# Performance work log

Measured on AMD Instinct MI355X. Metric: run time of the kernel, lower is better.

## Reference

```python
import jax, jax.numpy as jnp
from jax import lax
import numpy as np
import math

B, T, D_IN, H, L, NDIR = 32, 512, 1024, 512, 2, 2


def setup_inputs() -> dict:
    key = jax.random.key(0)
    ks = jax.random.split(key, 5)
    std = 1.0 / math.sqrt(H)  # torch init: uniform(-std, std)
    u = lambda k, shape: jax.random.uniform(k, shape, jnp.float32, -std, std)
    return {
        "x": jax.random.normal(ks[0], (B, T, D_IN), jnp.float32),
        "Wx": u(ks[1], (L, NDIR, D_IN, 4 * H)),   # x2h weight (in, 4H)
        "bx": u(ks[2], (L, NDIR, 4 * H)),
        "Wh": u(ks[3], (L, NDIR, H, 4 * H)),      # h2h weight (H, 4H)
        "bh": u(ks[4], (L, NDIR, 4 * H)),
    }


def _lstm_dir(xs, Wx, bx, Wh, bh):
    """xs: [T,B,Din]; returns hs [T,B,H], (hT, cT)."""
    # precompute input projection for all timesteps (one big GEMM)
    gx = jnp.einsum('tbd,dg->tbg', xs, Wx) + bx + bh  # [T,B,4H]
    h0 = jnp.zeros((xs.shape[1], Wh.shape[0]), xs.dtype)

    def step(carry, gx_t):
        h, c = carry
        gates = gx_t + h @ Wh  # [B,4H]
        i, f, g, o = jnp.split(gates, 4, axis=-1)  # torch chunk order: i,f,g,o
        i = jax.nn.sigmoid(i)
        f = jax.nn.sigmoid(f)
        g = jnp.tanh(g)
        o = jax.nn.sigmoid(o)
        c = c * f + i * g
        h = o * jnp.tanh(c)
        return (h, c), h

    (hT, cT), hs = lax.scan(step, (h0, h0), gx)
    return hs, hT, cT


def reference(x, Wx, bx, Wh, bh):
    # x: [B,T,D_IN] (batch_first) -> time-major
    inputs = jnp.swapaxes(x, 0, 1)  # [T,B,D]
    h_list, c_list = [], []
    for layer in range(L):
        outs_dirs = []
        for d in range(NDIR):
            xs = inputs if d == 0 else inputs[::-1]
            hs, hT, cT = _lstm_dir(xs, Wx[layer, d], bx[layer, d], Wh[layer, d], bh[layer, d])
            outs_dirs.append(hs if d == 0 else hs[::-1])
            h_list.append(hT)
            c_list.append(cT)
        inputs = jnp.concatenate(outs_dirs, axis=-1)  # [T,B,2H] (dropout=0 / eval)
    output = jnp.swapaxes(inputs, 0, 1)  # [B,T,2H]
    h_n = jnp.stack(h_list)  # [L*NDIR, B, H]
    c_n = jnp.stack(c_list)
    return output, h_n, c_n
```

## Files before the change

### kernel.cpp

```cpp
#include <hip/hip_runtime.h>
#include <hip/hip_bf16.h>

#define DEV __device__ __forceinline__

typedef __bf16 bf16;
typedef __bf16 bf16x8 __attribute__((ext_vector_type(8)));
typedef float f32x4 __attribute__((ext_vector_type(4)));
typedef int i32x4 __attribute__((ext_vector_type(4)));
typedef unsigned int u32;
typedef unsigned long long u64;

#define BB 32
#define TT 512
#define DIN 1024
#define HH 512
#define G4 2048
#define MM (TT*BB)

DEV float sigmf(float x){ return 1.0f/(1.0f + __expf(-x)); }
DEV float tanhfast(float x){ return 1.0f - 2.0f/(__expf(2.0f*x)+1.0f); }

DEV void gload16(const void* g, void* l){
  __builtin_amdgcn_global_load_lds((const __attribute__((address_space(1))) void*)g,
                                   (__attribute__((address_space(3))) void*)l, 16, 0, 0);
}

DEV i32x4 cload16(const void* p){
  i32x4 v;
  asm volatile("global_load_dwordx4 %0, %1, off sc0 sc1"
               : "=&v"(v) : "v"(p) : "memory");
  return v;
}
DEV void cstore8(void* p, u64 v){
  asm volatile("global_store_dwordx2 %0, %1, off sc0 sc1"
               :: "v"(p), "v"(v) : "memory");
}
DEV void waitvm0(){ asm volatile("s_waitcnt vmcnt(0)" ::: "memory"); }

__global__ void k_dbg(float* out, float v){ out[0] = v; }

__global__ void k_prep_bias(const float* __restrict__ bx, const float* __restrict__ bh,
                            float* __restrict__ bsum){
  int gid = blockIdx.x*256 + threadIdx.x;
  if (gid < 4*G4) bsum[gid] = bx[gid] + bh[gid];
}

__global__ void k_xswz(const float* __restrict__ x, bf16* __restrict__ xs){
  int gid = blockIdx.x*256 + threadIdx.x;
  int r = gid >> 7, kc = gid & 127;
  int b = r & 31, t = r >> 5;
  const float* px = x + ((size_t)b*TT + t)*DIN + kc*8;
  float4 v0 = *(const float4*)px;
  float4 v1 = *(const float4*)(px+4);
  bf16x8 o;
  o[0]=(bf16)v0.x; o[1]=(bf16)v0.y; o[2]=(bf16)v0.z; o[3]=(bf16)v0.w;
  o[4]=(bf16)v1.x; o[5]=(bf16)v1.y; o[6]=(bf16)v1.z; o[7]=(bf16)v1.w;
  *(bf16x8*)(xs + (size_t)r*DIN + ((kc ^ (r&7))<<3)) = o;
}

__global__ void k_twx(const float* __restrict__ Wx, bf16* __restrict__ Wxt){
  int ld = blockIdx.z;
  int k0 = blockIdx.x*64, n0 = blockIdx.y*64;
  const float* in = Wx + (size_t)ld*DIN*G4;
  bf16* outp = Wxt + (size_t)ld*G4*DIN;
  __shared__ float tile[64][68];
  int tid = threadIdx.x;
  #pragma unroll
  for (int rr=0; rr<4; rr++){
    int row = rr*16 + (tid>>4); int c4 = (tid&15)*4;
    float4 v = *(const float4*)(in + (size_t)(k0+row)*G4 + n0 + c4);
    *(float4*)&tile[row][c4] = v;
  }
  __syncthreads();
  #pragma unroll
  for (int uu=0; uu<2; uu++){
    int u = uu*256 + tid;
    int nn = u>>3, ck = u&7;
    bf16x8 o;
    #pragma unroll
    for (int j=0;j<8;j++) o[j] = (bf16)tile[ck*8+j][nn];
    int ncol = n0 + nn;
    int kcg = (k0>>3) + ck;
    *(bf16x8*)(outp + (size_t)ncol*DIN + ((size_t)(kcg ^ (ncol&7))<<3)) = o;
  }
}

__global__ void k_twh(const float* __restrict__ Wh, bf16* __restrict__ Whb){
  int ld = blockIdx.z;
  int k0 = blockIdx.x*64, n0 = blockIdx.y*64;
  const float* in = Wh + (size_t)ld*HH*G4;
  bf16* outp = Whb + (size_t)ld*G4*HH;
  __shared__ float tile[64][68];
  int tid = threadIdx.x;
  #pragma unroll
  for (int rr=0; rr<4; rr++){
    int row = rr*16 + (tid>>4); int c4 = (tid&15)*4;
    float4 v = *(const float4*)(in + (size_t)(k0+row)*G4 + n0 + c4);
    *(float4*)&tile[row][c4] = v;
  }
  __syncthreads();
  #pragma unroll
  for (int uu=0; uu<2; uu++){
    int u = uu*256 + tid;
    int nn = u>>3, ck = u&7;
    bf16x8 o;
    #pragma unroll
    for (int j=0;j<8;j++) o[j] = (bf16)tile[ck*8+j][nn];
    int n = n0 + nn;
    int q = n >> 9, rem = n & 511;
    int s = rem >> 4, wq = (rem >> 2) & 3, hcv = rem & 3;
    int cc = s*64 + wq*16 + q*4 + hcv;
    *(bf16x8*)(outp + (size_t)cc*HH + k0 + ck*8) = o;
  }
}

__launch_bounds__(256, 1)
__global__ void k_gemmp(const bf16* __restrict__ A, const bf16* __restrict__ Bw,
                        const float* __restrict__ bias, bf16* __restrict__ out){
  int d = blockIdx.z;
  const bf16* Bp = Bw + (size_t)d*G4*DIN;
  const float* bp = bias + d*G4;
  bf16* op = out + (size_t)d*MM*G4;
  int n0 = blockIdx.x*128, r0 = blockIdx.y*128;
  int tid = threadIdx.x, lane = tid&63, w = tid>>6;
  __shared__ __align__(16) bf16 ldsA[128*64];
  __shared__ __align__(16) bf16 ldsB[128*64];
  f32x4 acc[4][4];
  #pragma unroll
  for (int i=0;i<4;i++)
    #pragma unroll
    for (int j=0;j<4;j++) acc[i][j] = (f32x4){0.f,0.f,0.f,0.f};
  int wm = w>>1, wn = w&1;
  for (int kt=0; kt<16; kt++){
    __syncthreads();
    #pragma unroll
    for (int p=0;p<4;p++){
      int seg = p*4 + w;
      int row = seg*8 + (lane>>3);
      int cch = lane&7;
      gload16(A  + (size_t)(r0+row)*DIN + kt*64 + cch*8, ldsA + seg*512);
      gload16(Bp + (size_t)(n0+row)*DIN + kt*64 + cch*8, ldsB + seg*512);
    }
    __syncthreads();
    #pragma unroll
    for (int ks=0; ks<2; ks++){
      bf16x8 af[4], bf_[4];
      #pragma unroll
      for (int at=0; at<4; at++){
        int row = wm*64 + at*16 + (lane&15);
        int ch = (ks*4 + (lane>>4)) ^ (row&7);
        af[at] = *(const bf16x8*)(ldsA + row*64 + ch*8);
      }
      #pragma unroll
      for (int bt=0; bt<4; bt++){
        int col = wn*64 + bt*16 + (lane&15);
        int ch = (ks*4 + (lane>>4)) ^ (col&7);
        bf_[bt] = *(const bf16x8*)(ldsB + col*64 + ch*8);
      }
      #pragma unroll
      for (int at=0; at<4; at++)
        #pragma unroll
        for (int bt=0; bt<4; bt++)
          acc[at][bt] = __builtin_amdgcn_mfma_f32_16x16x32_bf16(af[at], bf_[bt], acc[at][bt], 0,0,0);
    }
  }
  float bv[4];
  #pragma unroll
  for (int bt=0;bt<4;bt++) bv[bt] = bp[n0 + wn*64 + bt*16 + (lane&15)];
  int l4 = lane>>4;
  #pragma unroll
  for (int a=0; a<2; a++){
    int tt = (r0 + wm*64 + a*32) >> 5;
    #pragma unroll
    for (int bt=0; bt<4; bt++){
      int col = n0 + wn*64 + bt*16 + (lane&15);
      int q = col >> 9, rem = col & 511;
      int sD = rem >> 4, wR = (rem >> 2) & 3, hcD = rem & 3;
      int tIdx = wR*64 + l4*16 + q*4 + hcD;
      bf16x8 u8;
      #pragma unroll
      for (int j=0;j<4;j++) u8[j]   = (bf16)(acc[a*2][bt][j]   + bv[bt]);
      #pragma unroll
      for (int j=0;j<4;j++) u8[4+j] = (bf16)(acc[a*2+1][bt][j] + bv[bt]);
      *(bf16x8*)(op + (((size_t)tt*32 + sD)*256 + tIdx)*8) = u8;
    }
  }
}

__launch_bounds__(256, 1)
__global__ void k_rec(const bf16* __restrict__ Whb, const bf16* __restrict__ gx,
                      char* __restrict__ hbS, bf16* __restrict__ out0,
                      float* __restrict__ dout,
                      float* __restrict__ hn, float* __restrict__ cn, int layer){
  int tid = threadIdx.x, lane = tid&63, w = tid>>6;
  int d = blockIdx.x >> 5, s = blockIdx.x & 31;
  __shared__ __align__(16) bf16 hA[32*512];
  __shared__ __align__(8) unsigned short hP[4*128];
  const bf16* Wp = Whb + ((size_t)d*G4 + s*64 + w*16 + (lane&15))*HH;
  bf16x8 bfr[16];
  #pragma unroll
  for (int kk=0; kk<16; kk++) bfr[kk] = *(const bf16x8*)(Wp + kk*32 + (lane>>4)*8);
  float cst[2][4] = {{0,0,0,0},{0,0,0,0}};
  const bf16* gxD = gx + (size_t)d*MM*G4;
  int q = (lane>>2)&3, hc = lane&3;
  int m0 = lane&15;
  bool hi = (q >= 2), odd = (q & 1);

  for (int t=0; t<TT; t++){
    int tt = d ? (TT-1-t) : t;
    bf16x8 gv = *(const bf16x8*)(gxD + (((size_t)tt*32 + s)*256 + tid)*8);
    f32x4 acc0 = {0.f,0.f,0.f,0.f}, acc1 = {0.f,0.f,0.f,0.f};
    if (t > 0){
      const char* sS = hbS + ((size_t)(d*TT + (t-1)) << 15);
      i32x4 u[8];
      #pragma unroll
      for (int i=0;i<8;i++) u[i] = cload16(sS + ((size_t)(i*256 + tid) << 4));
      waitvm0();
      __builtin_amdgcn_sched_barrier(0);
      u32 valid = 0;
      #pragma unroll
      for (int i=0;i<8;i++){
        bool ok = (u[i].x != -1) && (u[i].y != -1) && (u[i].z != -1) && (u[i].w != -1);
        valid |= (ok ? 1u : 0u) << i;
      }
      while (__any(valid != 0xFFu)){
        __builtin_amdgcn_s_sleep(1);
        #pragma unroll
        for (int i=0;i<8;i++)
          if (!((valid>>i)&1)) u[i] = cload16(sS + ((size_t)(i*256 + tid) << 4));
        waitvm0();
        __builtin_amdgcn_sched_barrier(0);
        valid = 0;
        #pragma unroll
        for (int i=0;i<8;i++){
          bool ok = (u[i].x != -1) && (u[i].y != -1) && (u[i].z != -1) && (u[i].w != -1);
          valid |= (ok ? 1u : 0u) << i;
        }
      }
      __syncthreads();
      #pragma unroll
      for (int i=0;i<8;i++){
        int g = i*256 + tid; int row = g>>6, uc = g&63;
        *(i32x4*)((char*)hA + row*1024 + ((uc ^ (row&7))<<4)) = u[i];
      }
      __syncthreads();
      #pragma unroll
      for (int kk=0; kk<16; kk++){
        int ch = (kk*4 + (lane>>4)) ^ (m0&7);
        bf16x8 a0 = *(const bf16x8*)(hA + m0*HH + ch*8);
        bf16x8 a1 = *(const bf16x8*)(hA + (m0+16)*HH + ch*8);
        acc0 = __builtin_amdgcn_mfma_f32_16x16x32_bf16(a0, bfr[kk], acc0, 0,0,0);
        acc1 = __builtin_amdgcn_mfma_f32_16x16x32_bf16(a1, bfr[kk], acc1, 0,0,0);
      }
    }
    #pragma unroll
    for (int mt=0; mt<2; mt++){
      #pragma unroll
      for (int rg=0; rg<4; rg++){
        float gpre = (mt ? acc1[rg] : acc0[rg]) + (float)gv[mt*4+rg];
        float x4  = __shfl_xor(gpre, 4);
        float x8  = __shfl_xor(gpre, 8);
        float x12 = __shfl_xor(gpre, 12);
        float a04 = odd ? x4 : gpre,  b04 = odd ? gpre : x4;
        float a812 = odd ? x12 : x8,  b812 = odd ? x8 : x12;
        float ig = hi ? a812 : a04;
        float fg = hi ? b812 : b04;
        float gg = hi ? a04 : a812;
        float og = hi ? b04 : b812;
        float iv = sigmf(ig), fv = sigmf(fg), gv_ = tanhfast(gg), ov = sigmf(og);
        float c = cst[mt][rg]*fv + iv*gv_;
        cst[mt][rg] = c;
        float hvv = ov * tanhfast(c);
        if (q == 0){
          int b = mt*16 + (lane>>4)*4 + rg;
          hP[w*128 + b*4 + hc] = __builtin_bit_cast(unsigned short, (bf16)hvv);
          if (layer == 1)
            __builtin_nontemporal_store(hvv,
              dout + ((size_t)(b*TT + tt))*(2*HH) + d*HH + s*16 + w*4 + hc);
          if (t == TT-1)
            hn[((size_t)((layer*2+d)*BB + b))*HH + s*16 + w*4 + hc] = hvv;
        }
      }
    }
    if (t == TT-1 && q == 0){
      #pragma unroll
      for (int mt=0; mt<2; mt++)
        #pragma unroll
        for (int rg=0; rg<4; rg++){
          int b = mt*16 + (lane>>4)*4 + rg;
          cn[((size_t)((layer*2+d)*BB + b))*HH + s*16 + w*4 + hc] = cst[mt][rg];
        }
    }
    if (lane < 32){
      u64 d8 = *(const u64*)(hP + w*128 + lane*4);
      if (t < TT-1)
        cstore8(hbS + ((size_t)(d*TT + t) << 15) + (((size_t)lane*128 + s*4 + w) << 3), d8);
      if (layer == 0){
        int r = tt*BB + lane;
        int c = d*64 + s*2 + (w>>1);
        *(u64*)(out0 + (size_t)r*DIN + (size_t)(c ^ (r&7))*8 + (w&1)*4) = d8;
      }
    }
  }
}

extern "C" void kernel_launch(void* const* d_in, const int* in_sizes, int n_in,
                              void* d_out, int out_size, void* d_ws, size_t ws_size,
                              hipStream_t stream){
  const float* x  = (const float*)d_in[0];
  const float* Wx = (const float*)d_in[1];
  const float* bx = (const float*)d_in[2];
  const float* Wh = (const float*)d_in[3];
  const float* bh = (const float*)d_in[4];
  float* outp = (float*)d_out;
  char* ws = (char*)d_ws;

  const size_t szWxt  = (size_t)4*G4*DIN*2;
  const size_t szWhb  = (size_t)4*G4*HH*2;
  const size_t szBsum = (size_t)4*G4*4;
  const size_t szXO   = (size_t)MM*DIN*2;
  const size_t szHbS  = (size_t)2*TT*32768;
  const size_t szGx   = (size_t)2*MM*G4*2;

  size_t off = 0;
  auto take = [&](size_t b)->size_t{ size_t r = off; off = (off + b + 255) & ~(size_t)255; return r; };
  size_t oWxt = take(szWxt), oWhb = take(szWhb), oBsum = take(szBsum);
  size_t oXO  = take(szXO), oHbS = take(szHbS), oGx = take(szGx);
  if (off > ws_size){
    k_dbg<<<1, 1, 0, stream>>>(outp, (float)((double)ws_size / 1048576.0));
    return;
  }

  bf16* Wxt  = (bf16*)(ws + oWxt);
  bf16* Whb  = (bf16*)(ws + oWhb);
  float* bsum= (float*)(ws + oBsum);
  bf16* xo   = (bf16*)(ws + oXO);
  bf16* out0 = xo;
  char* hbS  = ws + oHbS;
  bf16* gx   = (bf16*)(ws + oGx);

  float* hn = outp + (size_t)BB*TT*2*HH;
  float* cn = hn + (size_t)4*BB*HH;

  k_prep_bias<<<32, 256, 0, stream>>>(bx, bh, bsum);
  k_xswz<<<(MM*128)/256, 256, 0, stream>>>(x, xo);
  k_twx<<<dim3(16,32,4), 256, 0, stream>>>(Wx, Wxt);
  k_twh<<<dim3(8,32,4), 256, 0, stream>>>(Wh, Whb);

  for (int layer=0; layer<2; layer++){
    hipMemsetAsync(hbS, 0xFF, szHbS, stream);
    const bf16* A = layer ? out0 : xo;
    k_gemmp<<<dim3(16,128,2), 256, 0, stream>>>(A, Wxt + (size_t)layer*2*G4*DIN,
                                                bsum + layer*2*G4, gx);
    k_rec<<<64, 256, 0, stream>>>(Whb + (size_t)layer*2*G4*HH, gx, hbS, out0,
                                  outp, hn, cn, layer);
  }
}
```

Baseline: 5.939 ms.

## Merge four recurrent slices per 1024-thread block and batch output stores

The recurrent LSTM kernel now runs 16 blocks of 1024 threads instead of 64 blocks of 256. Each block covers four hidden slices, so the previous-step hidden state is polled and staged into shared memory once per four slices, and fewer blocks take part in the cross-block flag handshake. Per-step output writes (the bf16 layer-0 activations and the fp32 final output) go into a shared buffer and are flushed every 8 steps as wider stores. This adds per-CU serial work, costs more for each 1024-thread barrier and adds an extra barrier every 8 steps. The final-layer output is now rebuilt from bf16-rounded values, which loses some precision.

```diff
diff --git a/kernel.cpp b/kernel.cpp
--- a/kernel.cpp
+++ b/kernel.cpp
@@ -187,16 +187,19 @@
   }
 }
 
-__launch_bounds__(256, 1)
+__launch_bounds__(1024, 4)
 __global__ void k_rec(const bf16* __restrict__ Whb, const bf16* __restrict__ gx,
                       char* __restrict__ hbS, bf16* __restrict__ out0,
                       float* __restrict__ dout,
                       float* __restrict__ hn, float* __restrict__ cn, int layer){
-  int tid = threadIdx.x, lane = tid&63, w = tid>>6;
-  int d = blockIdx.x >> 5, s = blockIdx.x & 31;
+  int tidp = threadIdx.x, lane = tidp&63, w = tidp>>6;
+  int d = blockIdx.x >> 3, wg = blockIdx.x & 7;
+  int s = wg*4 + (w>>2);
+  int wq = w & 3;
   __shared__ __align__(16) bf16 hA[32*512];
-  __shared__ __align__(8) unsigned short hP[4*128];
-  const bf16* Wp = Whb + ((size_t)d*G4 + s*64 + w*16 + (lane&15))*HH;
+  __shared__ __align__(8) unsigned short hP[16*128];
+  __shared__ __align__(8) u64 outbuf[8][32][16];
+  const bf16* Wp = Whb + ((size_t)d*G4 + s*64 + wq*16 + (lane&15))*HH;
   bf16x8 bfr[16];
   #pragma unroll
   for (int kk=0; kk<16; kk++) bfr[kk] = *(const bf16x8*)(Wp + kk*32 + (lane>>4)*8);
@@ -208,39 +211,39 @@
 
   for (int t=0; t<TT; t++){
     int tt = d ? (TT-1-t) : t;
-    bf16x8 gv = *(const bf16x8*)(gxD + (((size_t)tt*32 + s)*256 + tid)*8);
+    bf16x8 gv = *(const bf16x8*)(gxD + (((size_t)tt*32 + s)*256 + (wq*64 + lane))*8);
     f32x4 acc0 = {0.f,0.f,0.f,0.f}, acc1 = {0.f,0.f,0.f,0.f};
     if (t > 0){
       const char* sS = hbS + ((size_t)(d*TT + (t-1)) << 15);
-      i32x4 u[8];
-      #pragma unroll
-      for (int i=0;i<8;i++) u[i] = cload16(sS + ((size_t)(i*256 + tid) << 4));
+      i32x4 u[2];
+      #pragma unroll
+      for (int i=0;i<2;i++) u[i] = cload16(sS + ((size_t)(i*1024 + tidp) << 4));
       waitvm0();
       __builtin_amdgcn_sched_barrier(0);
       u32 valid = 0;
       #pragma unroll
-      for (int i=0;i<8;i++){
+      for (int i=0;i<2;i++){
         bool ok = (u[i].x != -1) && (u[i].y != -1) && (u[i].z != -1) && (u[i].w != -1);
         valid |= (ok ? 1u : 0u) << i;
       }
-      while (__any(valid != 0xFFu)){
+      while (__any(valid != 3u)){
         __builtin_amdgcn_s_sleep(1);
         #pragma unroll
-        for (int i=0;i<8;i++)
-          if (!((valid>>i)&1)) u[i] = cload16(sS + ((size_t)(i*256 + tid) << 4));
+        for (int i=0;i<2;i++)
+          if (!((valid>>i)&1)) u[i] = cload16(sS + ((size_t)(i*1024 + tidp) << 4));
         waitvm0();
         __builtin_amdgcn_sched_barrier(0);
         valid = 0;
         #pragma unroll
-        for (int i=0;i<8;i++){
+        for (int i=0;i<2;i++){
           bool ok = (u[i].x != -1) && (u[i].y != -1) && (u[i].z != -1) && (u[i].w != -1);
           valid |= (ok ? 1u : 0u) << i;
         }
       }
       __syncthreads();
       #pragma unroll
-      for (int i=0;i<8;i++){
-        int g = i*256 + tid; int row = g>>6, uc = g&63;
+      for (int i=0;i<2;i++){
+        int g = i*1024 + tidp; int row = g>>6, uc = g&63;
         *(i32x4*)((char*)hA + row*1024 + ((uc ^ (row&7))<<4)) = u[i];
       }
       __syncthreads();
@@ -274,11 +277,8 @@
         if (q == 0){
           int b = mt*16 + (lane>>4)*4 + rg;
           hP[w*128 + b*4 + hc] = __builtin_bit_cast(unsigned short, (bf16)hvv);
-          if (layer == 1)
-            __builtin_nontemporal_store(hvv,
-              dout + ((size_t)(b*TT + tt))*(2*HH) + d*HH + s*16 + w*4 + hc);
           if (t == TT-1)
-            hn[((size_t)((layer*2+d)*BB + b))*HH + s*16 + w*4 + hc] = hvv;
+            hn[((size_t)((layer*2+d)*BB + b))*HH + s*16 + wq*4 + hc] = hvv;
         }
       }
     }
@@ -288,17 +288,39 @@
         #pragma unroll
         for (int rg=0; rg<4; rg++){
           int b = mt*16 + (lane>>4)*4 + rg;
-          cn[((size_t)((layer*2+d)*BB + b))*HH + s*16 + w*4 + hc] = cst[mt][rg];
+          cn[((size_t)((layer*2+d)*BB + b))*HH + s*16 + wq*4 + hc] = cst[mt][rg];
         }
     }
     if (lane < 32){
       u64 d8 = *(const u64*)(hP + w*128 + lane*4);
       if (t < TT-1)
-        cstore8(hbS + ((size_t)(d*TT + t) << 15) + (((size_t)lane*128 + s*4 + w) << 3), d8);
-      if (layer == 0){
-        int r = tt*BB + lane;
-        int c = d*64 + s*2 + (w>>1);
-        *(u64*)(out0 + (size_t)r*DIN + (size_t)(c ^ (r&7))*8 + (w&1)*4) = d8;
+        cstore8(hbS + ((size_t)(d*TT + t) << 15) + (((size_t)lane*128 + s*4 + wq) << 3), d8);
+      outbuf[t&7][lane][w] = d8;
+    }
+    if ((t&7) == 7){
+      __syncthreads();
+      int tbase = t - 7;
+      #pragma unroll
+      for (int k2=0; k2<4; k2++){
+        int u2 = k2*1024 + tidp;
+        int st = u2>>9, rem = u2&511, b = rem>>4, un = rem&15;
+        int tl = tbase + st;
+        int ttl = d ? (TT-1-tl) : tl;
+        u64 d8 = outbuf[st][b][un];
+        int s2 = wg*4 + (un>>2), w2 = un&3;
+        if (layer == 0){
+          int r = ttl*BB + b;
+          int c = d*64 + s2*2 + (w2>>1);
+          *(u64*)(out0 + (size_t)r*DIN + (size_t)(c ^ (r&7))*8 + (w2&1)*4) = d8;
+        } else {
+          const unsigned short* hp2 = (const unsigned short*)&d8;
+          float4 f;
+          f.x = __builtin_bit_cast(float, (u32)hp2[0] << 16);
+          f.y = __builtin_bit_cast(float, (u32)hp2[1] << 16);
+          f.z = __builtin_bit_cast(float, (u32)hp2[2] << 16);
+          f.w = __builtin_bit_cast(float, (u32)hp2[3] << 16);
+          *(float4*)(dout + ((size_t)(b*TT + ttl))*(2*HH) + d*HH + s2*16 + w2*4) = f;
+        }
       }
     }
   }
@@ -352,7 +374,7 @@
     const bf16* A = layer ? out0 : xo;
     k_gemmp<<<dim3(16,128,2), 256, 0, stream>>>(A, Wxt + (size_t)layer*2*G4*DIN,
                                                 bsum + layer*2*G4, gx);
-    k_rec<<<64, 256, 0, stream>>>(Whb + (size_t)layer*2*G4*HH, gx, hbS, out0,
-                                  outp, hn, cn, layer);
-  }
-}
+    k_rec<<<16, 1024, 0, stream>>>(Whb + (size_t)layer*2*G4*HH, gx, hbS, out0,
+                                   outp, hn, cn, layer);
+  }
+}
```

Result: slower. 13.50 ms (+127.3%).

## Load recurrent h fragments directly from global into MFMA registers, skipping LDS staging

Applied to the files above, without the earlier changes.

Each wave now loads the previous-step hidden state straight from the global staging buffer into MFMA A-operand registers in fragment layout, instead of cooperatively loading into registers, writing to swizzled LDS, and re-reading. This removes two block barriers and the LDS round trip from the serial per-timestep critical path. In exchange, every wave redundantly fetches the full 32x512 h tile, four times the global/L2 traffic per block. It also raises register pressure (32 vector registers of 16 bytes) and weakens the staleness check to two words per fragment.

```diff
diff --git a/kernel.cpp b/kernel.cpp
--- a/kernel.cpp
+++ b/kernel.cpp
@@ -194,7 +194,6 @@
                       float* __restrict__ hn, float* __restrict__ cn, int layer){
   int tid = threadIdx.x, lane = tid&63, w = tid>>6;
   int d = blockIdx.x >> 5, s = blockIdx.x & 31;
-  __shared__ __align__(16) bf16 hA[32*512];
   __shared__ __align__(8) unsigned short hP[4*128];
   const bf16* Wp = Whb + ((size_t)d*G4 + s*64 + w*16 + (lane&15))*HH;
   bf16x8 bfr[16];
@@ -205,6 +204,7 @@
   int q = (lane>>2)&3, hc = lane&3;
   int m0 = lane&15;
   bool hi = (q >= 2), odd = (q & 1);
+  int boff = m0*1024 + (lane>>4)*16;
 
   for (int t=0; t<TT; t++){
     int tt = d ? (TT-1-t) : t;
@@ -212,45 +212,42 @@
     f32x4 acc0 = {0.f,0.f,0.f,0.f}, acc1 = {0.f,0.f,0.f,0.f};
     if (t > 0){
       const char* sS = hbS + ((size_t)(d*TT + (t-1)) << 15);
-      i32x4 u[8];
-      #pragma unroll
-      for (int i=0;i<8;i++) u[i] = cload16(sS + ((size_t)(i*256 + tid) << 4));
+      i32x4 fa[16], fb[16];
+      #pragma unroll
+      for (int kk=0; kk<16; kk++){
+        fa[kk] = cload16(sS + boff + kk*64);
+        fb[kk] = cload16(sS + boff + 16384 + kk*64);
+      }
       waitvm0();
       __builtin_amdgcn_sched_barrier(0);
-      u32 valid = 0;
-      #pragma unroll
-      for (int i=0;i<8;i++){
-        bool ok = (u[i].x != -1) && (u[i].y != -1) && (u[i].z != -1) && (u[i].w != -1);
-        valid |= (ok ? 1u : 0u) << i;
-      }
-      while (__any(valid != 0xFFu)){
+      u32 stale = 0;
+      #pragma unroll
+      for (int kk=0; kk<16; kk++){
+        if (fa[kk].x == -1 || fa[kk].z == -1) stale |= 1u << kk;
+        if (fb[kk].x == -1 || fb[kk].z == -1) stale |= 1u << (16+kk);
+      }
+      while (__any(stale != 0)){
         __builtin_amdgcn_s_sleep(1);
         #pragma unroll
-        for (int i=0;i<8;i++)
-          if (!((valid>>i)&1)) u[i] = cload16(sS + ((size_t)(i*256 + tid) << 4));
+        for (int kk=0; kk<16; kk++){
+          if (stale & (1u<<kk))      fa[kk] = cload16(sS + boff + kk*64);
+          if (stale & (1u<<(16+kk))) fb[kk] = cload16(sS + boff + 16384 + kk*64);
+        }
         waitvm0();
         __builtin_amdgcn_sched_barrier(0);
-        valid = 0;
+        stale = 0;
         #pragma unroll
-        for (int i=0;i<8;i++){
-          bool ok = (u[i].x != -1) && (u[i].y != -1) && (u[i].z != -1) && (u[i].w != -1);
-          valid |= (ok ? 1u : 0u) << i;
+        for (int kk=0; kk<16; kk++){
+          if (fa[kk].x == -1 || fa[kk].z == -1) stale |= 1u << kk;
+          if (fb[kk].x == -1 || fb[kk].z == -1) stale |= 1u << (16+kk);
         }
       }
-      __syncthreads();
-      #pragma unroll
-      for (int i=0;i<8;i++){
-        int g = i*256 + tid; int row = g>>6, uc = g&63;
-        *(i32x4*)((char*)hA + row*1024 + ((uc ^ (row&7))<<4)) = u[i];
-      }
-      __syncthreads();
       #pragma unroll
       for (int kk=0; kk<16; kk++){
-        int ch = (kk*4 + (lane>>4)) ^ (m0&7);
-        bf16x8 a0 = *(const bf16x8*)(hA + m0*HH + ch*8);
-        bf16x8 a1 = *(const bf16x8*)(hA + (m0+16)*HH + ch*8);
-        acc0 = __builtin_amdgcn_mfma_f32_16x16x32_bf16(a0, bfr[kk], acc0, 0,0,0);
-        acc1 = __builtin_amdgcn_mfma_f32_16x16x32_bf16(a1, bfr[kk], acc1, 0,0,0);
+        acc0 = __builtin_amdgcn_mfma_f32_16x16x32_bf16(
+                 __builtin_bit_cast(bf16x8, fa[kk]), bfr[kk], acc0, 0,0,0);
+        acc1 = __builtin_amdgcn_mfma_f32_16x16x32_bf16(
+                 __builtin_bit_cast(bf16x8, fb[kk]), bfr[kk], acc1, 0,0,0);
       }
     }
     #pragma unroll
```

Result: slower. 11.55 ms (+94.5%).

## Merge both LSTM directions into one 512-thread block with per-direction LDS barriers

Applied to the files above, without the earlier changes.

The recurrent kernel now launches 32 blocks of 512 threads instead of 64 blocks of 256. Each block handles one column slice for both directions, four waves per direction. The two __syncthreads calls are replaced by per-direction named barriers built on LDS atomic counters with sleep-polling, so the two directions do not wait on each other. This halves the number of workgroups taking part in the cross-block spin-wait handoff of h and packs the two directions onto the same CUs. The cost is a heavier CU per block, twice the LDS, and software barriers that may carry more latency than hardware ones.

```diff
diff --git a/kernel.cpp b/kernel.cpp
--- a/kernel.cpp
+++ b/kernel.cpp
@@ -187,34 +187,44 @@
   }
 }
 
-__launch_bounds__(256, 1)
+__launch_bounds__(512, 2)
 __global__ void k_rec(const bf16* __restrict__ Whb, const bf16* __restrict__ gx,
                       char* __restrict__ hbS, bf16* __restrict__ out0,
                       float* __restrict__ dout,
                       float* __restrict__ hn, float* __restrict__ cn, int layer){
   int tid = threadIdx.x, lane = tid&63, w = tid>>6;
-  int d = blockIdx.x >> 5, s = blockIdx.x & 31;
-  __shared__ __align__(16) bf16 hA[32*512];
-  __shared__ __align__(8) unsigned short hP[4*128];
-  const bf16* Wp = Whb + ((size_t)d*G4 + s*64 + w*16 + (lane&15))*HH;
+  int d = w >> 2;
+  int wq = w & 3;
+  int tid_h = wq*64 + lane;
+  int s = blockIdx.x;
+  __shared__ __align__(16) bf16 hA[2][32*512];
+  __shared__ __align__(8) unsigned short hP[8*128];
+  __shared__ u32 bcnt[2];
+  if (tid < 2) bcnt[tid] = 0;
+  __syncthreads();
+
+  const bf16* Wp = Whb + ((size_t)d*G4 + s*64 + wq*16 + (lane&15))*HH;
   bf16x8 bfr[16];
   #pragma unroll
   for (int kk=0; kk<16; kk++) bfr[kk] = *(const bf16x8*)(Wp + kk*32 + (lane>>4)*8);
   float cst[2][4] = {{0,0,0,0},{0,0,0,0}};
   const bf16* gxD = gx + (size_t)d*MM*G4;
+  u32* myc = &bcnt[d];
+  bf16* hAd = hA[d];
+  u32 barseq = 0;
   int q = (lane>>2)&3, hc = lane&3;
   int m0 = lane&15;
   bool hi = (q >= 2), odd = (q & 1);
 
   for (int t=0; t<TT; t++){
     int tt = d ? (TT-1-t) : t;
-    bf16x8 gv = *(const bf16x8*)(gxD + (((size_t)tt*32 + s)*256 + tid)*8);
+    bf16x8 gv = *(const bf16x8*)(gxD + (((size_t)tt*32 + s)*256 + tid_h)*8);
     f32x4 acc0 = {0.f,0.f,0.f,0.f}, acc1 = {0.f,0.f,0.f,0.f};
     if (t > 0){
       const char* sS = hbS + ((size_t)(d*TT + (t-1)) << 15);
       i32x4 u[8];
       #pragma unroll
-      for (int i=0;i<8;i++) u[i] = cload16(sS + ((size_t)(i*256 + tid) << 4));
+      for (int i=0;i<8;i++) u[i] = cload16(sS + ((size_t)(i*256 + tid_h) << 4));
       waitvm0();
       __builtin_amdgcn_sched_barrier(0);
       u32 valid = 0;
@@ -227,7 +237,7 @@
         __builtin_amdgcn_s_sleep(1);
         #pragma unroll
         for (int i=0;i<8;i++)
-          if (!((valid>>i)&1)) u[i] = cload16(sS + ((size_t)(i*256 + tid) << 4));
+          if (!((valid>>i)&1)) u[i] = cload16(sS + ((size_t)(i*256 + tid_h) << 4));
         waitvm0();
         __builtin_amdgcn_sched_barrier(0);
         valid = 0;
@@ -237,18 +247,26 @@
           valid |= (ok ? 1u : 0u) << i;
         }
       }
-      __syncthreads();
+      barseq++;
+      if (lane == 0)
+        __hip_atomic_fetch_add(myc, 1u, __ATOMIC_RELEASE, __HIP_MEMORY_SCOPE_WORKGROUP);
+      while (__hip_atomic_load(myc, __ATOMIC_ACQUIRE, __HIP_MEMORY_SCOPE_WORKGROUP) < barseq*4u)
+        __builtin_amdgcn_s_sleep(1);
       #pragma unroll
       for (int i=0;i<8;i++){
-        int g = i*256 + tid; int row = g>>6, uc = g&63;
-        *(i32x4*)((char*)hA + row*1024 + ((uc ^ (row&7))<<4)) = u[i];
-      }
-      __syncthreads();
+        int g = i*256 + tid_h; int row = g>>6, uc = g&63;
+        *(i32x4*)((char*)hAd + row*1024 + ((uc ^ (row&7))<<4)) = u[i];
+      }
+      barseq++;
+      if (lane == 0)
+        __hip_atomic_fetch_add(myc, 1u, __ATOMIC_RELEASE, __HIP_MEMORY_SCOPE_WORKGROUP);
+      while (__hip_atomic_load(myc, __ATOMIC_ACQUIRE, __HIP_MEMORY_SCOPE_WORKGROUP) < barseq*4u)
+        __builtin_amdgcn_s_sleep(1);
       #pragma unroll
       for (int kk=0; kk<16; kk++){
         int ch = (kk*4 + (lane>>4)) ^ (m0&7);
-        bf16x8 a0 = *(const bf16x8*)(hA + m0*HH + ch*8);
-        bf16x8 a1 = *(const bf16x8*)(hA + (m0+16)*HH + ch*8);
+        bf16x8 a0 = *(const bf16x8*)(hAd + m0*HH + ch*8);
+        bf16x8 a1 = *(const bf16x8*)(hAd + (m0+16)*HH + ch*8);
         acc0 = __builtin_amdgcn_mfma_f32_16x16x32_bf16(a0, bfr[kk], acc0, 0,0,0);
         acc1 = __builtin_amdgcn_mfma_f32_16x16x32_bf16(a1, bfr[kk], acc1, 0,0,0);
       }
@@ -276,9 +294,9 @@
           hP[w*128 + b*4 + hc] = __builtin_bit_cast(unsigned short, (bf16)hvv);
           if (layer == 1)
             __builtin_nontemporal_store(hvv,
-              dout + ((size_t)(b*TT + tt))*(2*HH) + d*HH + s*16 + w*4 + hc);
+              dout + ((size_t)(b*TT + tt))*(2*HH) + d*HH + s*16 + wq*4 + hc);
           if (t == TT-1)
-            hn[((size_t)((layer*2+d)*BB + b))*HH + s*16 + w*4 + hc] = hvv;
+            hn[((size_t)((layer*2+d)*BB + b))*HH + s*16 + wq*4 + hc] = hvv;
         }
       }
     }
@@ -288,17 +306,17 @@
         #pragma unroll
         for (int rg=0; rg<4; rg++){
           int b = mt*16 + (lane>>4)*4 + rg;
-          cn[((size_t)((layer*2+d)*BB + b))*HH + s*16 + w*4 + hc] = cst[mt][rg];
+          cn[((size_t)((layer*2+d)*BB + b))*HH + s*16 + wq*4 + hc] = cst[mt][rg];
         }
     }
     if (lane < 32){
       u64 d8 = *(const u64*)(hP + w*128 + lane*4);
       if (t < TT-1)
-        cstore8(hbS + ((size_t)(d*TT + t) << 15) + (((size_t)lane*128 + s*4 + w) << 3), d8);
+        cstore8(hbS + ((size_t)(d*TT + t) << 15) + (((size_t)lane*128 + s*4 + wq) << 3), d8);
       if (layer == 0){
         int r = tt*BB + lane;
-        int c = d*64 + s*2 + (w>>1);
-        *(u64*)(out0 + (size_t)r*DIN + (size_t)(c ^ (r&7))*8 + (w&1)*4) = d8;
+        int c = d*64 + s*2 + (wq>>1);
+        *(u64*)(out0 + (size_t)r*DIN + (size_t)(c ^ (r&7))*8 + (wq&1)*4) = d8;
       }
     }
   }
@@ -352,7 +370,7 @@
     const bf16* A = layer ? out0 : xo;
     k_gemmp<<<dim3(16,128,2), 256, 0, stream>>>(A, Wxt + (size_t)layer*2*G4*DIN,
                                                 bsum + layer*2*G4, gx);
-    k_rec<<<64, 256, 0, stream>>>(Whb + (size_t)layer*2*G4*HH, gx, hbS, out0,
+    k_rec<<<32, 512, 0, stream>>>(Whb + (size_t)layer*2*G4*HH, gx, hbS, out0,
                                   outp, hn, cn, layer);
   }
 }
```

After: 8.125 ms. +36.8%, slower.
